# Kernel optimization log

Measured on AMD Instinct MI355X. Metric: run time of the kernel, lower is better.

## Reference

```python
import jax, jax.numpy as jnp
import numpy as np

EPS = 1e-11

def squash(s, axis=-1):
    sq = jnp.sum(s * s, axis=axis, keepdims=True)
    return (sq / (1.0 + sq)) * s / jnp.sqrt(sq + EPS)

def routing(u_hat, scale, num_iters=3):
    # u_hat: (b, P, J, D); dynamic routing (Sabour et al.), softmax over output capsules J
    b, P, J, D = u_hat.shape
    b_ij = jnp.zeros((b, P, J), u_hat.dtype)
    v = None
    for _ in range(num_iters):
        c = jax.nn.softmax(b_ij, axis=-1)
        s = jnp.einsum('bpj,bpjd->bjd', c, u_hat) / scale
        v = squash(s)
        b_ij = b_ij + jnp.einsum('bpjd,bjd->bpj', u_hat, v)
    return v

def normalize_adj(adj):
    deg = jnp.sum(adj, axis=-1)
    d_inv_sqrt = jnp.where(deg > 0, deg ** -0.5, 0.0)
    return d_inv_sqrt[:, :, None] * adj * d_inv_sqrt[:, None, :]

def setup_inputs():
    key = jax.random.key(0)
    ks = jax.random.split(key, 20)
    b, n = 32, 512
    vocabs = [128, 64, 16]
    emb, C, L = 64, 2, 3
    hidden = emb * C                 # 128
    gcn_in = emb * len(vocabs)       # 192
    att_dim = emb * C * L            # 384
    Jg, Dg = 16, 32                  # num_graph_capsules, graph_embedding_size
    ncls = 6
    recon_hidden = int(gcn_in * 2 / 3)  # 128
    recon_dim = 208
    g = lambda i, *s: jax.random.normal(ks[i], s, jnp.float32) * 0.05
    # sparse symmetric adjacency with self-loops (binary, like real graph data)
    adj = (jax.random.uniform(ks[0], (b, n, n)) < 0.02).astype(jnp.float32)
    adj = jnp.maximum(adj, jnp.swapaxes(adj, 1, 2))
    adj = jnp.maximum(adj, jnp.eye(n, dtype=jnp.float32)[None])
    return {
        'adj': adj,
        'nodes0': jax.random.randint(ks[1], (b, n), 0, vocabs[0]),
        'nodes1': jax.random.randint(ks[2], (b, n), 0, vocabs[1]),
        'nodes2': jax.random.randint(ks[3], (b, n), 0, vocabs[2]),
        'label': jax.random.randint(ks[4], (b,), 0, ncls),
        'reconstructs': jax.random.uniform(ks[5], (b, recon_dim)),
        'emb0': g(6, vocabs[0], emb), 'emb1': g(7, vocabs[1], emb), 'emb2': g(8, vocabs[2], emb),
        'gw0': g(9, gcn_in, hidden), 'gb0': jnp.zeros((hidden,), jnp.float32),
        'gw1': g(10, hidden, hidden), 'gb1': jnp.zeros((hidden,), jnp.float32),
        'gw2': g(11, hidden, hidden), 'gb2': jnp.zeros((hidden,), jnp.float32),
        'aw1': g(12, att_dim, att_dim), 'ab1': jnp.zeros((att_dim,), jnp.float32),
        'aw2': g(13, att_dim, 1), 'ab2': jnp.zeros((1,), jnp.float32),
        'Wg': g(14, C * L, emb, Jg, Dg),
        'Wc': g(15, Jg, Dg, ncls, Dg),
        'rw1': g(16, Dg, recon_hidden), 'rb1': jnp.zeros((recon_hidden,), jnp.float32),
        'rw2': g(17, recon_hidden, recon_dim), 'rb2': jnp.zeros((recon_dim,), jnp.float32),
    }

def reference(adj, nodes0, nodes1, nodes2, label, reconstructs,
              emb0, emb1, emb2, gw0, gb0, gw1, gb1, gw2, gb2,
              aw1, ab1, aw2, ab2, Wg, Wc, rw1, rb1, rw2, rb2):
    b, n, _ = adj.shape
    C = 2
    lambda_val, reg_scale = 0.5, 0.1
    # embeddings (dropout omitted: eval-mode reference)
    feats = jnp.concatenate([emb0[nodes0], emb1[nodes1], emb2[nodes2]], axis=-1)  # (b,n,192)
    masks = jnp.max(adj, axis=-1, keepdims=True)                    # (b,n,1)
    num_nodes = jnp.sum(masks, axis=1, keepdims=True)[..., None]    # (b,1,1,1)
    adj_norm = normalize_adj(adj)
    hid = []
    h = feats
    for W, bb in ((gw0, gb0), (gw1, gb1), (gw2, gb2)):
        h = jnp.tanh(jnp.einsum('bnm,bmd->bnd', adj_norm, h @ W + bb))
        hid.append(h.reshape(b, n, C, -1))
    H = jnp.concatenate(hid, axis=2)                                # (b,n,C*L,emb)
    attn = jnp.tanh(H.reshape(b, n, -1) @ aw1 + ab1) @ aw2 + ab2    # (b,n,1)
    attn = jax.nn.softmax(jnp.where(masks > 0, attn, -jnp.inf), axis=1)[..., None]
    H = H * attn * num_nodes
    # graph capsules: every (node, channel) is an input capsule
    Jg, Dg = Wg.shape[2], Wg.shape[3]
    u_hat = jnp.einsum('bnci,cijd->bncjd', H, Wg).reshape(b, n * Wg.shape[0], Jg, Dg)
    v_g = routing(u_hat, num_nodes.reshape(b, 1, 1))                # (b,Jg,Dg)
    u_hat2 = jnp.einsum('bci,cijd->bcjd', v_g, Wc)
    v_c = routing(u_hat2, 1.0)                                      # (b,ncls,Dg)
    # margin loss
    v_mag = jnp.sqrt(jnp.sum(v_c * v_c, axis=2))
    pred = jnp.argmax(v_mag, axis=1)
    max_l = jnp.maximum(0.9 - v_mag, 0.0) ** 2
    max_r = jnp.maximum(v_mag - 0.1, 0.0) ** 2
    T_c = jax.nn.one_hot(label, v_mag.shape[1], dtype=v_c.dtype)
    L_c = jnp.sum(T_c * max_l + lambda_val * (1.0 - T_c) * max_r, axis=1)
    margin_loss = jnp.mean(L_c)
    # reconstruction loss
    capsule_masked = jnp.sum(v_c * T_c[..., None], axis=1)          # (b,Dg)
    rec = jax.nn.sigmoid(jax.nn.relu(capsule_masked @ rw1 + rb1) @ rw2 + rb2)
    neg_ind = (reconstructs < 1e-05).astype(rec.dtype)
    pos_ind = 1.0 - neg_ind
    rec_val = reconstructs / (jnp.max(reconstructs, axis=1, keepdims=True) + EPS)
    diff = (rec - rec_val) ** 2
    recon_loss = jnp.mean(jnp.max(diff * pos_ind, axis=-1) + jnp.max(diff * neg_ind, axis=-1))
    loss = margin_loss + recon_loss * reg_scale
    return (v_c, loss, margin_loss, recon_loss, pred)
```

## Files before the change

### kernel.cpp

```cpp
#include <hip/hip_runtime.h>
#include <hip/hip_bf16.h>
#include <math.h>

#define NB 32
#define NN 512
#define GIN 192
#define ATT 384
#define EPSF 1e-11f

typedef __attribute__((ext_vector_type(4))) float f32x4;
typedef __attribute__((ext_vector_type(8))) short short8;

__device__ __forceinline__ ushort bfhi(float f) {
    uint u = __float_as_uint(f);
    return (ushort)((u + 0x7FFFu + ((u >> 16) & 1u)) >> 16);
}
__device__ __forceinline__ float bff(ushort h) {
    return __uint_as_float(((uint)h) << 16);
}
__device__ __forceinline__ void bfsplit(float f, ushort& hi, ushort& lo) {
    hi = bfhi(f);
    lo = bfhi(f - bff(hi));
}

__global__ __launch_bounds__(64) void k_prep(const float* __restrict__ adj,
                                             ushort* __restrict__ nbr,
                                             int* __restrict__ deg,
                                             float* __restrict__ dinv,
                                             float* __restrict__ mask) {
    int row = blockIdx.x;
    int t = threadIdx.x;
    const float* a = adj + (size_t)row * NN;
    float4 v0 = ((const float4*)a)[t * 2];
    float4 v1 = ((const float4*)a)[t * 2 + 1];
    float vv[8] = {v0.x, v0.y, v0.z, v0.w, v1.x, v1.y, v1.z, v1.w};
    float s = 0.f, m = 0.f;
    int cnt = 0;
    unsigned long long below = (t == 63) ? 0xFFFFFFFFFFFFFFFFULL >> 1
                                         : ((1ULL << t) - 1ULL);
#pragma unroll
    for (int e = 0; e < 8; e++) {
        float v = vv[e];
        s += v;
        m = fmaxf(m, v);
        bool nz = v != 0.f;
        unsigned long long bm = __ballot(nz);
        int pos = cnt + __popcll(bm & below);
        if (nz && pos < 64) nbr[(size_t)row * 64 + pos] = (ushort)(t * 8 + e);
        cnt += __popcll(bm);
    }
    for (int off = 32; off; off >>= 1) {
        s += __shfl_xor(s, off);
        m = fmaxf(m, __shfl_xor(m, off));
    }
    if (t == 0) {
        deg[row] = cnt < 64 ? cnt : 64;
        dinv[row] = s > 0.f ? 1.0f / sqrtf(s) : 0.f;
        mask[row] = m;
    }
}

__global__ void k_gather(const int* __restrict__ n0, const int* __restrict__ n1,
                         const int* __restrict__ n2, const float* __restrict__ e0,
                         const float* __restrict__ e1, const float* __restrict__ e2,
                         ushort* __restrict__ fh, ushort* __restrict__ fl) {
    int tid = blockIdx.x * 256 + threadIdx.x;
    if (tid >= NB * NN * GIN) return;
    int bn = tid / GIN, f = tid - bn * GIN;
    float v;
    if (f < 64)       v = e0[n0[bn] * 64 + f];
    else if (f < 128) v = e1[n1[bn] * 64 + (f - 64)];
    else              v = e2[n2[bn] * 64 + (f - 128)];
    ushort h, lo;
    bfsplit(v, h, lo);
    fh[tid] = h; fl[tid] = lo;
}

__global__ __launch_bounds__(256) void k_twtall(
    const float* __restrict__ gw0, const float* __restrict__ gw1,
    const float* __restrict__ gw2, const float* __restrict__ aw1,
    ushort* __restrict__ t0h, ushort* __restrict__ t0l,
    ushort* __restrict__ t1h, ushort* __restrict__ t1l,
    ushort* __restrict__ t2h, ushort* __restrict__ t2l,
    ushort* __restrict__ tah, ushort* __restrict__ tal) {
    const float* W; ushort *Th, *Tl; int K, N;
    switch (blockIdx.z) {
        case 0: W = gw0; Th = t0h; Tl = t0l; K = 192; N = 128; break;
        case 1: W = gw1; Th = t1h; Tl = t1l; K = 128; N = 128; break;
        case 2: W = gw2; Th = t2h; Tl = t2l; K = 128; N = 128; break;
        default: W = aw1; Th = tah; Tl = tal; K = 384; N = 384; break;
    }
    int k0 = blockIdx.x * 32, n0 = blockIdx.y * 32;
    if (k0 >= K || n0 >= N) return;
    __shared__ float tile[32][33];
    int t = threadIdx.x, tx = t & 31, ty = t >> 5;
#pragma unroll
    for (int r = 0; r < 4; r++)
        tile[ty + r * 8][tx] = W[(size_t)(k0 + ty + r * 8) * N + n0 + tx];
    __syncthreads();
#pragma unroll
    for (int r = 0; r < 4; r++) {
        int nn = ty + r * 8;
        float v = tile[tx][nn];
        ushort h, lo;
        bfsplit(v, h, lo);
        size_t o = (size_t)(n0 + nn) * K + k0 + tx;
        Th[o] = h; Tl[o] = lo;
    }
}

template <int KK, int EPI>
__global__ __launch_bounds__(256) void k_mfg(
    const ushort* __restrict__ Ah, const ushort* __restrict__ Al, int lda,
    const ushort* __restrict__ Bh, const ushort* __restrict__ Bl,
    const float* __restrict__ bias, const float* __restrict__ dinv,
    ushort* __restrict__ O1, ushort* __restrict__ O2, float* __restrict__ Of,
    const float* __restrict__ aw2p) {
    __shared__ ushort Ash[2048], Asl[2048];
    __shared__ ushort Bsh[4096], Bsl[4096];
    __shared__ float ep[(EPI == 0) ? 64 * 128 : 1];
    int t = threadIdx.x;
    int bid = blockIdx.x;
    {
        int q = gridDim.x >> 3;
        bid = (bid & 7) * q + (bid >> 3);
    }
    int m0 = bid * 64;
    int n0 = blockIdx.y * 128;
    int l = t & 63, w = t >> 6, wr = w >> 1, wc = w & 1;
    int rA = t >> 2, kc = t & 3;
    int rB0 = rA, rB1 = rA + 64;
    int lsA  = ((rA >> 4) * 64 + (rA & 15) + kc * 16) * 8;
    int lsB0 = ((rB0 >> 4) * 64 + (rB0 & 15) + kc * 16) * 8;
    int lsB1 = ((rB1 >> 4) * 64 + (rB1 & 15) + kc * 16) * 8;
    f32x4 z = {0.f, 0.f, 0.f, 0.f};
    f32x4 acc[2][4];
#pragma unroll
    for (int i = 0; i < 2; i++)
#pragma unroll
        for (int j = 0; j < 4; j++) acc[i][j] = z;

    short8 pa0, pal0, pb0, pb1, pbl0, pbl1;
    int kof = kc * 8;
    {
        pa0 = *(const short8*)&Ah[(size_t)(m0 + rA) * lda + kof];
        pal0 = *(const short8*)&Al[(size_t)(m0 + rA) * lda + kof];
        pb0 = *(const short8*)&Bh[(size_t)(n0 + rB0) * KK + kof];
        pb1 = *(const short8*)&Bh[(size_t)(n0 + rB1) * KK + kof];
        pbl0 = *(const short8*)&Bl[(size_t)(n0 + rB0) * KK + kof];
        pbl1 = *(const short8*)&Bl[(size_t)(n0 + rB1) * KK + kof];
    }
    for (int k0 = 0; k0 < KK; k0 += 32) {
        *(short8*)&Ash[lsA] = pa0;
        *(short8*)&Asl[lsA] = pal0;
        *(short8*)&Bsh[lsB0] = pb0;
        *(short8*)&Bsh[lsB1] = pb1;
        *(short8*)&Bsl[lsB0] = pbl0;
        *(short8*)&Bsl[lsB1] = pbl1;
        __syncthreads();
        if (k0 + 32 < KK) {
            int kn = k0 + 32 + kof;
            pa0 = *(const short8*)&Ah[(size_t)(m0 + rA) * lda + kn];
            pal0 = *(const short8*)&Al[(size_t)(m0 + rA) * lda + kn];
            pb0 = *(const short8*)&Bh[(size_t)(n0 + rB0) * KK + kn];
            pb1 = *(const short8*)&Bh[(size_t)(n0 + rB1) * KK + kn];
            pbl0 = *(const short8*)&Bl[(size_t)(n0 + rB0) * KK + kn];
            pbl1 = *(const short8*)&Bl[(size_t)(n0 + rB1) * KK + kn];
        }
        short8 ah[2], al[2], bh[4], bl[4];
#pragma unroll
        for (int i = 0; i < 2; i++) {
            ah[i] = *(const short8*)&Ash[((wr * 2 + i) * 64 + l) * 8];
            al[i] = *(const short8*)&Asl[((wr * 2 + i) * 64 + l) * 8];
        }
#pragma unroll
        for (int j = 0; j < 4; j++) {
            bh[j] = *(const short8*)&Bsh[((wc * 4 + j) * 64 + l) * 8];
            bl[j] = *(const short8*)&Bsl[((wc * 4 + j) * 64 + l) * 8];
        }
#pragma unroll
        for (int i = 0; i < 2; i++)
#pragma unroll
            for (int j = 0; j < 4; j++) {
                acc[i][j] = __builtin_amdgcn_mfma_f32_16x16x32_bf16(ah[i], bh[j], acc[i][j], 0, 0, 0);
                acc[i][j] = __builtin_amdgcn_mfma_f32_16x16x32_bf16(ah[i], bl[j], acc[i][j], 0, 0, 0);
                acc[i][j] = __builtin_amdgcn_mfma_f32_16x16x32_bf16(al[i], bh[j], acc[i][j], 0, 0, 0);
            }
        __syncthreads();
    }
    if constexpr (EPI == 3) {
#pragma unroll
        for (int i = 0; i < 2; i++) {
            float rs[4] = {0.f, 0.f, 0.f, 0.f};
#pragma unroll
            for (int j = 0; j < 4; j++) {
                int gc = n0 + (wc * 4 + j) * 16 + (l & 15);
                float bv = bias[gc], wv = aw2p[gc];
#pragma unroll
                for (int r = 0; r < 4; r++)
                    rs[r] += tanhf(acc[i][j][r] + bv) * wv;
            }
#pragma unroll
            for (int r = 0; r < 4; r++) {
                rs[r] += __shfl_xor(rs[r], 1, 16);
                rs[r] += __shfl_xor(rs[r], 2, 16);
                rs[r] += __shfl_xor(rs[r], 4, 16);
                rs[r] += __shfl_xor(rs[r], 8, 16);
            }
            if ((l & 15) == 0) {
                int gr0 = m0 + (wr * 2 + i) * 16 + 4 * (l >> 4);
#pragma unroll
                for (int r = 0; r < 4; r++) atomicAdd(&Of[gr0 + r], rs[r]);
            }
        }
    } else {
#pragma unroll
        for (int i = 0; i < 2; i++)
#pragma unroll
            for (int j = 0; j < 4; j++) {
                int lc = (wc * 4 + j) * 16 + (l & 15);
                int lr0 = (wr * 2 + i) * 16 + 4 * (l >> 4);
                float bv = bias[lc];
#pragma unroll
                for (int r = 0; r < 4; r++)
                    ep[(lr0 + r) * 128 + lc] = (acc[i][j][r] + bv) * dinv[m0 + lr0 + r];
            }
        __syncthreads();
        int row = t >> 2, c0 = (t & 3) * 32;
        ushort hs[32], lsv[32];
#pragma unroll
        for (int c = 0; c < 32; c++) bfsplit(ep[row * 128 + c0 + c], hs[c], lsv[c]);
        size_t ob = (size_t)(m0 + row) * 128 + c0;
#pragma unroll
        for (int k = 0; k < 4; k++) {
            *(short8*)&O1[ob + k * 8] = *(const short8*)&hs[k * 8];
            *(short8*)&O2[ob + k * 8] = *(const short8*)&lsv[k * 8];
        }
    }
}

__global__ __launch_bounds__(256) void k_adjsp(const ushort* __restrict__ nbr,
                                               const int* __restrict__ deg,
                                               const ushort* __restrict__ Yh,
                                               const ushort* __restrict__ Yl,
                                               const float* __restrict__ dinv,
                                               ushort* __restrict__ Hbh,
                                               ushort* __restrict__ Hbl, int hoff) {
    int bid = blockIdx.x;
    {
        int q = gridDim.x >> 3;
        bid = (bid & 7) * q + (bid >> 3);
    }
    int b = bid >> 3, rb = bid & 7;
    int base = b * NN + rb * 64;
    __shared__ ushort nl[64 * 64];
    __shared__ int dl[64];
    int t = threadIdx.x;
    *(short8*)&nl[t * 16] = *(const short8*)&nbr[(size_t)base * 64 + t * 16];
    *(short8*)&nl[t * 16 + 8] = *(const short8*)&nbr[(size_t)base * 64 + t * 16 + 8];
    if (t < 64) dl[t] = deg[base + t];
    __syncthreads();
    int row = t >> 2, c0 = (t & 3) * 32;
    const ushort* yhp = Yh + (size_t)b * 65536 + c0;
    const ushort* ylp = Yl + (size_t)b * 65536 + c0;
    float acc[32];
#pragma unroll
    for (int c = 0; c < 32; c++) acc[c] = 0.f;
    int dg = dl[row];
    for (int q = 0; q < dg; q++) {
        int m = nl[row * 64 + q];
        const short8* yh = (const short8*)(yhp + m * 128);
        const short8* yl = (const short8*)(ylp + m * 128);
        short8 h0 = yh[0], h1 = yh[1], h2 = yh[2], h3 = yh[3];
        short8 l0 = yl[0], l1 = yl[1], l2 = yl[2], l3 = yl[3];
#pragma unroll
        for (int k = 0; k < 8; k++) {
            acc[k]      += bff((ushort)h0[k]) + bff((ushort)l0[k]);
            acc[8 + k]  += bff((ushort)h1[k]) + bff((ushort)l1[k]);
            acc[16 + k] += bff((ushort)h2[k]) + bff((ushort)l2[k]);
            acc[24 + k] += bff((ushort)h3[k]) + bff((ushort)l3[k]);
        }
    }
    float dv = dinv[base + row];
    ushort hs[32], lsv[32];
#pragma unroll
    for (int c = 0; c < 32; c++) {
        float v = tanhf(acc[c] * dv);
        bfsplit(v, hs[c], lsv[c]);
    }
    size_t o = (size_t)(base + row) * ATT + hoff + c0;
#pragma unroll
    for (int k = 0; k < 4; k++) {
        *(short8*)&Hbh[o + k * 8] = *(const short8*)&hs[k * 8];
        *(short8*)&Hbl[o + k * 8] = *(const short8*)&lsv[k * 8];
    }
}

__global__ __launch_bounds__(512) void k_attnsm(float* __restrict__ logit,
                                                const float* __restrict__ mask,
                                                float* __restrict__ numn) {
    __shared__ float red[8], red2[8], red3[8];
    int b = blockIdx.x, t = threadIdx.x;
    float mk = mask[b * NN + t];
    float x = mk > 0.f ? logit[b * NN + t] : -INFINITY;
    float m = x, nsum = mk;
    for (int off = 32; off; off >>= 1) {
        m = fmaxf(m, __shfl_xor(m, off));
        nsum += __shfl_xor(nsum, off);
    }
    if ((t & 63) == 0) { red[t >> 6] = m; red3[t >> 6] = nsum; }
    __syncthreads();
    float gm = red[0], nn = red3[0];
    for (int i = 1; i < 8; i++) { gm = fmaxf(gm, red[i]); nn += red3[i]; }
    float e = expf(x - gm);
    float s = e;
    for (int off = 32; off; off >>= 1) s += __shfl_xor(s, off);
    if ((t & 63) == 0) red2[t >> 6] = s;
    __syncthreads();
    float gs = 0.f;
    for (int i = 0; i < 8; i++) gs += red2[i];
    logit[b * NN + t] = (e / gs) * nn;
    if (t == 0) numn[b] = nn;
}

__global__ __launch_bounds__(256) void k_Hsum(const ushort* __restrict__ Hh,
                                              const ushort* __restrict__ Hl,
                                              const float* __restrict__ scale,
                                              float* __restrict__ G0) {
    int blk = blockIdx.x;
    int c = blk % 6, b = blk / 6;
    int t = threadIdx.x;
    int i = t & 63, g = t >> 6;
    float s = 0.f;
    for (int n = g * 128; n < g * 128 + 128; n++) {
        size_t o = ((size_t)b * NN + n) * ATT + c * 64 + i;
        s += scale[b * NN + n] * (bff(Hh[o]) + bff(Hl[o]));
    }
    __shared__ float red[256];
    red[t] = s;
    __syncthreads();
    if (t < 128) red[t] += red[t + 128];
    __syncthreads();
    if (t < 64) G0[(size_t)blk * 64 + i] = red[t] + red[t + 64];
}

template <int SRC, bool DOWV>
__global__ __launch_bounds__(256) void k_SVj(const float* __restrict__ gsrc,
                                             const float* __restrict__ Wg,
                                             const float* __restrict__ numn,
                                             float* __restrict__ vg,
                                             float* __restrict__ Wv) {
    int b = blockIdx.x, j = blockIdx.y;
    int t = threadIdx.x;
    __shared__ float Wgl[384 * 33];
    __shared__ float gj[384];
    __shared__ float red[256];
    __shared__ float vvs[32];
    for (int idx = t; idx < 12288; idx += 256) {
        int r = idx >> 5, d = idx & 31;
        Wgl[r * 33 + d] = Wg[(size_t)r * 512 + j * 32 + d];
    }
    for (int r = t; r < 384; r += 256) {
        if constexpr (SRC == 0) {
            gj[r] = gsrc[b * 384 + r] * (1.f / 16.f);
        } else {
            const float* g = gsrc + ((size_t)b * 6 + (r >> 6)) * 4096 + j * 64 + (r & 63);
            gj[r] = g[0] + g[1024] + g[2048] + g[3072];
        }
    }
    __syncthreads();
    int d = t & 31, g8 = t >> 5;
    float pp = 0.f;
#pragma unroll
    for (int k = 0; k < 48; k++) {
        int r = g8 * 48 + k;
        pp += gj[r] * Wgl[r * 33 + d];
    }
    red[t] = pp;
    __syncthreads();
    if (t < 128) red[t] += red[t + 128];
    __syncthreads();
    if (t < 64) red[t] += red[t + 64];
    __syncthreads();
    if (t < 32) {
        float s = (red[t] + red[t + 32]) / numn[b];
        float sq = s * s;
        for (int off = 16; off; off >>= 1) sq += __shfl_xor(sq, off, 32);
        float v = (sq / (1.f + sq)) * s / sqrtf(sq + EPSF);
        vvs[t] = v;
        vg[(size_t)b * 512 + j * 32 + t] = v;
    }
    __syncthreads();
    if constexpr (DOWV) {
        for (int r = t; r < 384; r += 256) {
            float a = 0.f;
#pragma unroll
            for (int d2 = 0; d2 < 32; d2++) a += Wgl[r * 33 + d2] * vvs[d2];
            Wv[(size_t)b * 6144 + (r >> 6) * 1024 + (r & 63) * 16 + j] = a;
        }
    }
}

__global__ __launch_bounds__(256) void k_GsSM(const float* __restrict__ bij,
                                              const ushort* __restrict__ Hh,
                                              const ushort* __restrict__ Hl,
                                              const float* __restrict__ scale,
                                              float* __restrict__ Gs) {
    int blk = blockIdx.x;
    int seg = blk & 3, c = (blk >> 2) % 6, b = blk / 24;
    __shared__ float ct[16 * 16];
    __shared__ float ht[16 * 64];
    int t = threadIdx.x;
    int i = t & 63, j0 = t >> 6;
    float acc[4] = {0.f, 0.f, 0.f, 0.f};
    int n0 = seg * 128;
    for (int nc = 0; nc < 128; nc += 16) {
        {
            int nn = t >> 4;
            float v = bij[(((size_t)b * NN + n0 + nc + nn) * 6 + c) * 16 + (t & 15)];
            float mx = v;
            mx = fmaxf(mx, __shfl_xor(mx, 1, 16));
            mx = fmaxf(mx, __shfl_xor(mx, 2, 16));
            mx = fmaxf(mx, __shfl_xor(mx, 4, 16));
            mx = fmaxf(mx, __shfl_xor(mx, 8, 16));
            float e = expf(v - mx);
            float sm = e;
            sm += __shfl_xor(sm, 1, 16);
            sm += __shfl_xor(sm, 2, 16);
            sm += __shfl_xor(sm, 4, 16);
            sm += __shfl_xor(sm, 8, 16);
            ct[t] = e / sm;
        }
        for (int idx = t; idx < 1024; idx += 256) {
            int nn = idx >> 6, ii = idx & 63;
            int n = n0 + nc + nn;
            size_t o = ((size_t)b * NN + n) * ATT + c * 64 + ii;
            ht[idx] = scale[b * NN + n] * (bff(Hh[o]) + bff(Hl[o]));
        }
        __syncthreads();
        for (int nn = 0; nn < 16; nn++) {
            float hv = ht[nn * 64 + i];
#pragma unroll
            for (int q = 0; q < 4; q++) acc[q] += ct[nn * 16 + j0 * 4 + q] * hv;
        }
        __syncthreads();
    }
#pragma unroll
    for (int q = 0; q < 4; q++) {
        int j = j0 * 4 + q;
        Gs[(((size_t)b * 6 + c) * 4 + seg) * 1024 + j * 64 + i] = acc[q];
    }
}

template <bool ACC>
__global__ __launch_bounds__(256) void k_bup(const ushort* __restrict__ Hh,
                                             const ushort* __restrict__ Hl,
                                             const float* __restrict__ scale,
                                             const float* __restrict__ Wv,
                                             float* __restrict__ bij) {
    int blk = blockIdx.x;
    int b = blk >> 4;
    int n0 = (blk & 15) * 32;
    __shared__ float wl[6144];
    __shared__ float hl[32 * ATT];
    int t = threadIdx.x;
    for (int idx = t; idx < 6144; idx += 256) wl[idx] = Wv[(size_t)b * 6144 + idx];
    for (int idx = t; idx < 32 * ATT; idx += 256) {
        int nn = idx / ATT;
        size_t o = ((size_t)b * NN + n0) * ATT + idx;
        hl[idx] = scale[b * NN + n0 + nn] * (bff(Hh[o]) + bff(Hl[o]));
    }
    __syncthreads();
    for (int idx = t; idx < 3072; idx += 256) {
        int nn = idx / 96, r = idx % 96, c = r >> 4, j = r & 15;
        float a = 0.f;
        const float* h = hl + nn * ATT + c * 64;
        const float* w = wl + c * 1024 + j;
#pragma unroll
        for (int i2 = 0; i2 < 64; i2++) a += h[i2] * w[i2 * 16];
        size_t o = (((size_t)b * NN + n0 + nn) * 6 + c) * 16 + j;
        if constexpr (ACC) bij[o] += a;
        else bij[o] = a;
    }
}

__global__ __launch_bounds__(256) void k_u2(const float* __restrict__ vg,
                                            const float* __restrict__ Wc,
                                            float* __restrict__ u2g) {
    int c = blockIdx.x;
    int t = threadIdx.x;
    __shared__ float Wcl[32 * 192];
    __shared__ float vgl[32 * 32];
    for (int idx = t; idx < 6144; idx += 256)
        Wcl[idx] = Wc[(size_t)c * 6144 + idx];
    for (int idx = t; idx < 1024; idx += 256) {
        int b = idx >> 5, i2 = idx & 31;
        vgl[idx] = vg[(size_t)b * 512 + c * 32 + i2];
    }
    __syncthreads();
    for (int o = t; o < 6144; o += 256) {
        int b = o / 192, jd = o - b * 192;
        float a = 0.f;
#pragma unroll
        for (int i2 = 0; i2 < 32; i2++) a += vgl[b * 32 + i2] * Wcl[i2 * 192 + jd];
        u2g[(size_t)b * 3072 + c * 192 + jd] = a;
    }
}

__global__ __launch_bounds__(256) void k_caps2(
    const float* __restrict__ u2g,
    const int* __restrict__ label, const float* __restrict__ recon_in,
    const float* __restrict__ rw1, const float* __restrict__ rb1,
    const float* __restrict__ rw2, const float* __restrict__ rb2,
    float* __restrict__ out, float* __restrict__ marg, float* __restrict__ reconl) {
    int b = blockIdx.x, t = threadIdx.x;
    __shared__ float u2[3072];
    __shared__ float b2[96], c2b[96];
    __shared__ float vv[192];
    __shared__ float magl[6];
    __shared__ float cm[32];
    __shared__ float hidl[128];
    __shared__ float red[256];
    for (int idx = t; idx < 3072; idx += 256) u2[idx] = u2g[(size_t)b * 3072 + idx];
    if (t < 96) b2[t] = 0.f;
    __syncthreads();
    for (int it = 0; it < 3; it++) {
        if (t < 16) {
            float mx = -INFINITY;
            for (int j = 0; j < 6; j++) mx = fmaxf(mx, b2[t * 6 + j]);
            float e[6], s = 0.f;
            for (int j = 0; j < 6; j++) { e[j] = expf(b2[t * 6 + j] - mx); s += e[j]; }
            for (int j = 0; j < 6; j++) c2b[t * 6 + j] = e[j] / s;
        }
        __syncthreads();
        if (t < 192) {
            int j = t >> 5, d = t & 31;
            float s = 0.f;
            for (int c = 0; c < 16; c++) s += c2b[c * 6 + j] * u2[c * 192 + j * 32 + d];
            float sq = s * s;
            for (int off = 16; off; off >>= 1) sq += __shfl_xor(sq, off, 32);
            vv[t] = (sq / (1.f + sq)) * s / sqrtf(sq + EPSF);
        }
        __syncthreads();
        if (it < 2) {
            if (t < 96) {
                int c = t / 6, j = t - c * 6;
                float a = 0.f;
                for (int d = 0; d < 32; d++) a += u2[c * 192 + j * 32 + d] * vv[j * 32 + d];
                b2[t] += a;
            }
            __syncthreads();
        }
    }
    if (t < 192) out[(size_t)b * 192 + t] = vv[t];
    if (t < 6) {
        float s = 0.f;
        for (int d = 0; d < 32; d++) { float v = vv[t * 32 + d]; s += v * v; }
        magl[t] = sqrtf(s);
    }
    __syncthreads();
    int lab = label[b];
    if (t == 0) {
        float L = 0.f;
        int p = 0;
        float best = magl[0];
        for (int j = 0; j < 6; j++) {
            float mg = magl[j];
            if (mg > best) { best = mg; p = j; }
            float ml = fmaxf(0.9f - mg, 0.f); ml *= ml;
            float mr = fmaxf(mg - 0.1f, 0.f); mr *= mr;
            L += (j == lab) ? ml : 0.5f * mr;
        }
        marg[b] = L;
        out[6147 + b] = (float)p;
    }
    if (t < 32) cm[t] = vv[lab * 32 + t];
    __syncthreads();
    if (t < 128) {
        float a = rb1[t];
        for (int d = 0; d < 32; d++) a += cm[d] * rw1[d * 128 + t];
        hidl[t] = fmaxf(a, 0.f);
    }
    __syncthreads();
    bool act = t < 208;
    float rv = 0.f, rin = 0.f;
    if (act) {
        float a = rb2[t];
        for (int k = 0; k < 128; k++) a += hidl[k] * rw2[k * 208 + t];
        rv = 1.f / (1.f + expf(-a));
        rin = recon_in[(size_t)b * 208 + t];
    }
    red[t] = act ? rin : -INFINITY;
    __syncthreads();
    for (int s2 = 128; s2; s2 >>= 1) {
        if (t < s2) red[t] = fmaxf(red[t], red[t + s2]);
        __syncthreads();
    }
    float rmax = red[0];
    __syncthreads();
    float dpos = 0.f, dneg = 0.f;
    if (act) {
        float rec_val = rin / (rmax + EPSF);
        float d2 = rv - rec_val; d2 *= d2;
        bool neg = rin < 1e-5f;
        dpos = neg ? 0.f : d2;
        dneg = neg ? d2 : 0.f;
    }
    red[t] = dpos;
    __syncthreads();
    for (int s2 = 128; s2; s2 >>= 1) {
        if (t < s2) red[t] = fmaxf(red[t], red[t + s2]);
        __syncthreads();
    }
    float mp = red[0];
    __syncthreads();
    red[t] = dneg;
    __syncthreads();
    for (int s2 = 128; s2; s2 >>= 1) {
        if (t < s2) red[t] = fmaxf(red[t], red[t + s2]);
        __syncthreads();
    }
    if (t == 0) reconl[b] = mp + red[0];
}

__global__ void k_final(const float* __restrict__ marg, const float* __restrict__ reconl,
                        float* __restrict__ out) {
    int t = threadIdx.x;
    float m = (t < 32) ? marg[t] : 0.f;
    float r = (t < 32) ? reconl[t] : 0.f;
    for (int off = 16; off; off >>= 1) { m += __shfl_xor(m, off, 32); r += __shfl_xor(r, off, 32); }
    if (t == 0) {
        m /= 32.f;
        r /= 32.f;
        out[6144] = m + 0.1f * r;
        out[6145] = m;
        out[6146] = r;
    }
}

extern "C" void kernel_launch(void* const* d_in, const int* in_sizes, int n_in,
                              void* d_out, int out_size, void* d_ws, size_t ws_size,
                              hipStream_t stream) {
    const float* adj   = (const float*)d_in[0];
    const int*   n0    = (const int*)d_in[1];
    const int*   n1    = (const int*)d_in[2];
    const int*   n2    = (const int*)d_in[3];
    const int*   label = (const int*)d_in[4];
    const float* recon = (const float*)d_in[5];
    const float* e0    = (const float*)d_in[6];
    const float* e1    = (const float*)d_in[7];
    const float* e2    = (const float*)d_in[8];
    const float* gw0   = (const float*)d_in[9];
    const float* gb0   = (const float*)d_in[10];
    const float* gw1   = (const float*)d_in[11];
    const float* gb1   = (const float*)d_in[12];
    const float* gw2   = (const float*)d_in[13];
    const float* gb2   = (const float*)d_in[14];
    const float* aw1   = (const float*)d_in[15];
    const float* ab1   = (const float*)d_in[16];
    const float* aw2   = (const float*)d_in[17];
    const float* Wg    = (const float*)d_in[19];
    const float* Wc    = (const float*)d_in[20];
    const float* rw1   = (const float*)d_in[21];
    const float* rb1   = (const float*)d_in[22];
    const float* rw2   = (const float*)d_in[23];
    const float* rb2   = (const float*)d_in[24];
    float* out = (float*)d_out;

    char* p = (char*)d_ws;
    auto alloc = [&](size_t bytes) { char* r = p; p += (bytes + 255) & ~(size_t)255; return r; };
    float*  dinv   = (float*)alloc(NB * NN * 4);
    float*  maskp  = (float*)alloc(NB * NN * 4);
    float*  numn   = (float*)alloc(NB * 4);
    float*  logit  = (float*)alloc(NB * NN * 4);
    float*  bij    = (float*)alloc((size_t)NB * NN * 96 * 4);
    float*  Gs     = (float*)alloc((size_t)NB * 24576 * 4);
    float*  G0     = (float*)alloc(NB * 384 * 4);
    float*  vg     = (float*)alloc(NB * 512 * 4);
    float*  Wv     = (float*)alloc(NB * 6144 * 4);
    float*  u2g    = (float*)alloc(NB * 3072 * 4);
    float*  marg   = (float*)alloc(NB * 4);
    float*  recl   = (float*)alloc(NB * 4);
    int*    deg    = (int*)alloc(NB * NN * 4);
    ushort* nbr    = (ushort*)alloc((size_t)NB * NN * 64 * 2);
    ushort* gwt0h  = (ushort*)alloc(128 * 192 * 2);
    ushort* gwt0l  = (ushort*)alloc(128 * 192 * 2);
    ushort* gwt1h  = (ushort*)alloc(128 * 128 * 2);
    ushort* gwt1l  = (ushort*)alloc(128 * 128 * 2);
    ushort* gwt2h  = (ushort*)alloc(128 * 128 * 2);
    ushort* gwt2l  = (ushort*)alloc(128 * 128 * 2);
    ushort* aw1th  = (ushort*)alloc(384 * 384 * 2);
    ushort* aw1tl  = (ushort*)alloc(384 * 384 * 2);
    ushort* Yth    = (ushort*)alloc((size_t)NB * NN * 128 * 2);
    ushort* Ytl    = (ushort*)alloc((size_t)NB * NN * 128 * 2);
    ushort* Hbh    = (ushort*)alloc((size_t)NB * NN * ATT * 2);
    ushort* Hbl    = (ushort*)alloc((size_t)NB * NN * ATT * 2);
    ushort* fbh    = (ushort*)alloc((size_t)NB * NN * GIN * 2);
    ushort* fbl    = (ushort*)alloc((size_t)NB * NN * GIN * 2);

    k_prep<<<NB * NN, 64, 0, stream>>>(adj, nbr, deg, dinv, maskp);
    k_gather<<<(NB * NN * GIN + 255) / 256, 256, 0, stream>>>(n0, n1, n2, e0, e1, e2, fbh, fbl);
    k_twtall<<<dim3(12, 12, 4), 256, 0, stream>>>(gw0, gw1, gw2, aw1, gwt0h, gwt0l,
                                                  gwt1h, gwt1l, gwt2h, gwt2l, aw1th, aw1tl);

    k_mfg<192, 0><<<256, 256, 0, stream>>>(fbh, fbl, 192, gwt0h, gwt0l, gb0, dinv,
                                           Yth, Ytl, nullptr, nullptr);
    k_adjsp<<<256, 256, 0, stream>>>(nbr, deg, Yth, Ytl, dinv, Hbh, Hbl, 0);
    k_mfg<128, 0><<<256, 256, 0, stream>>>(Hbh, Hbl, ATT, gwt1h, gwt1l, gb1, dinv,
                                           Yth, Ytl, nullptr, nullptr);
    k_adjsp<<<256, 256, 0, stream>>>(nbr, deg, Yth, Ytl, dinv, Hbh, Hbl, 128);
    k_mfg<128, 0><<<256, 256, 0, stream>>>(Hbh + 128, Hbl + 128, ATT, gwt2h, gwt2l, gb2, dinv,
                                           Yth, Ytl, nullptr, nullptr);
    k_adjsp<<<256, 256, 0, stream>>>(nbr, deg, Yth, Ytl, dinv, Hbh, Hbl, 256);

    hipMemsetAsync(logit, 0, NB * NN * sizeof(float), stream);
    k_mfg<384, 3><<<dim3(256, 3), 256, 0, stream>>>(Hbh, Hbl, ATT, aw1th, aw1tl, ab1, nullptr,
                                                    nullptr, nullptr, logit, aw2);
    k_attnsm<<<NB, 512, 0, stream>>>(logit, maskp, numn);

    k_Hsum<<<NB * 6, 256, 0, stream>>>(Hbh, Hbl, logit, G0);
    k_SVj<0, true><<<dim3(NB, 16), 256, 0, stream>>>(G0, Wg, numn, vg, Wv);
    k_bup<false><<<NB * 16, 256, 0, stream>>>(Hbh, Hbl, logit, Wv, bij);
    k_GsSM<<<NB * 24, 256, 0, stream>>>(bij, Hbh, Hbl, logit, Gs);
    k_SVj<1, true><<<dim3(NB, 16), 256, 0, stream>>>(Gs, Wg, numn, vg, Wv);
    k_bup<true><<<NB * 16, 256, 0, stream>>>(Hbh, Hbl, logit, Wv, bij);
    k_GsSM<<<NB * 24, 256, 0, stream>>>(bij, Hbh, Hbl, logit, Gs);
    k_SVj<1, false><<<dim3(NB, 16), 256, 0, stream>>>(Gs, Wg, numn, vg, nullptr);

    k_u2<<<16, 256, 0, stream>>>(vg, Wc, u2g);
    k_caps2<<<NB, 256, 0, stream>>>(u2g, label, recon, rw1, rb1, rw2, rb2, out, marg, recl);
    k_final<<<1, 64, 0, stream>>>(marg, recl, out);
}
```

Before: 440.3 us.

## Store GCN intermediate Y as fp32 and re-split sparse aggregation into finer blocks

The GEMM epilogue now writes the intermediate Y directly as fp32 instead of splitting it into bf16 hi/lo pairs, and the sparse adjacency aggregation reads one fp32 array instead of two bf16 arrays. The aggregation kernel is also re-partitioned into 16 rows per block with 16 threads per row and 8 columns each, quadrupling the grid to 1024 blocks. This removes split/recombine arithmetic, gives each gather coalesced 32-byte reads per thread, and adds parallelism to hide gather latency. The byte count of Y is unchanged, and the smaller blocks reload neighbor lists per block.

```diff
diff --git a/kernel.cpp b/kernel.cpp
--- a/kernel.cpp
+++ b/kernel.cpp
@@ -114,8 +114,7 @@
     const ushort* __restrict__ Ah, const ushort* __restrict__ Al, int lda,
     const ushort* __restrict__ Bh, const ushort* __restrict__ Bl,
     const float* __restrict__ bias, const float* __restrict__ dinv,
-    ushort* __restrict__ O1, ushort* __restrict__ O2, float* __restrict__ Of,
-    const float* __restrict__ aw2p) {
+    float* __restrict__ Of, const float* __restrict__ aw2p) {
     __shared__ ushort Ash[2048], Asl[2048];
     __shared__ ushort Bsh[4096], Bsl[4096];
     __shared__ float ep[(EPI == 0) ? 64 * 128 : 1];
@@ -227,22 +226,16 @@
             }
         __syncthreads();
         int row = t >> 2, c0 = (t & 3) * 32;
-        ushort hs[32], lsv[32];
-#pragma unroll
-        for (int c = 0; c < 32; c++) bfsplit(ep[row * 128 + c0 + c], hs[c], lsv[c]);
         size_t ob = (size_t)(m0 + row) * 128 + c0;
 #pragma unroll
-        for (int k = 0; k < 4; k++) {
-            *(short8*)&O1[ob + k * 8] = *(const short8*)&hs[k * 8];
-            *(short8*)&O2[ob + k * 8] = *(const short8*)&lsv[k * 8];
-        }
+        for (int k = 0; k < 8; k++)
+            ((float4*)&Of[ob])[k] = *(const float4*)&ep[row * 128 + c0 + k * 4];
     }
 }
 
 __global__ __launch_bounds__(256) void k_adjsp(const ushort* __restrict__ nbr,
                                                const int* __restrict__ deg,
-                                               const ushort* __restrict__ Yh,
-                                               const ushort* __restrict__ Yl,
+                                               const float* __restrict__ Y,
                                                const float* __restrict__ dinv,
                                                ushort* __restrict__ Hbh,
                                                ushort* __restrict__ Hbl, int hoff) {
@@ -251,49 +244,38 @@
         int q = gridDim.x >> 3;
         bid = (bid & 7) * q + (bid >> 3);
     }
-    int b = bid >> 3, rb = bid & 7;
-    int base = b * NN + rb * 64;
-    __shared__ ushort nl[64 * 64];
-    __shared__ int dl[64];
-    int t = threadIdx.x;
-    *(short8*)&nl[t * 16] = *(const short8*)&nbr[(size_t)base * 64 + t * 16];
-    *(short8*)&nl[t * 16 + 8] = *(const short8*)&nbr[(size_t)base * 64 + t * 16 + 8];
-    if (t < 64) dl[t] = deg[base + t];
-    __syncthreads();
-    int row = t >> 2, c0 = (t & 3) * 32;
-    const ushort* yhp = Yh + (size_t)b * 65536 + c0;
-    const ushort* ylp = Yl + (size_t)b * 65536 + c0;
-    float acc[32];
-#pragma unroll
-    for (int c = 0; c < 32; c++) acc[c] = 0.f;
+    int b = bid >> 5;
+    int rg = bid & 31;
+    int base = b * NN + rg * 16;
+    __shared__ ushort nl[16 * 64];
+    __shared__ int dl[16];
+    int t = threadIdx.x;
+    if (t < 128) *(short8*)&nl[t * 8] = *(const short8*)&nbr[(size_t)base * 64 + t * 8];
+    if (t < 16) dl[t] = deg[base + t];
+    __syncthreads();
+    int row = t >> 4, c0 = (t & 15) * 8;
+    const float* yp = Y + (size_t)b * 65536 + c0;
+    float acc[8] = {0.f, 0.f, 0.f, 0.f, 0.f, 0.f, 0.f, 0.f};
     int dg = dl[row];
+    const ushort* nr = &nl[row * 64];
     for (int q = 0; q < dg; q++) {
-        int m = nl[row * 64 + q];
-        const short8* yh = (const short8*)(yhp + m * 128);
-        const short8* yl = (const short8*)(ylp + m * 128);
-        short8 h0 = yh[0], h1 = yh[1], h2 = yh[2], h3 = yh[3];
-        short8 l0 = yl[0], l1 = yl[1], l2 = yl[2], l3 = yl[3];
-#pragma unroll
-        for (int k = 0; k < 8; k++) {
-            acc[k]      += bff((ushort)h0[k]) + bff((ushort)l0[k]);
-            acc[8 + k]  += bff((ushort)h1[k]) + bff((ushort)l1[k]);
-            acc[16 + k] += bff((ushort)h2[k]) + bff((ushort)l2[k]);
-            acc[24 + k] += bff((ushort)h3[k]) + bff((ushort)l3[k]);
-        }
+        const float4* y = (const float4*)(yp + (int)nr[q] * 128);
+        float4 a = y[0], c = y[1];
+        acc[0] += a.x; acc[1] += a.y; acc[2] += a.z; acc[3] += a.w;
+        acc[4] += c.x; acc[5] += c.y; acc[6] += c.z; acc[7] += c.w;
     }
     float dv = dinv[base + row];
-    ushort hs[32], lsv[32];
-#pragma unroll
-    for (int c = 0; c < 32; c++) {
+    short8 vh, vl;
+#pragma unroll
+    for (int c = 0; c < 8; c++) {
         float v = tanhf(acc[c] * dv);
-        bfsplit(v, hs[c], lsv[c]);
+        ushort h, lo;
+        bfsplit(v, h, lo);
+        vh[c] = (short)h; vl[c] = (short)lo;
     }
     size_t o = (size_t)(base + row) * ATT + hoff + c0;
-#pragma unroll
-    for (int k = 0; k < 4; k++) {
-        *(short8*)&Hbh[o + k * 8] = *(const short8*)&hs[k * 8];
-        *(short8*)&Hbl[o + k * 8] = *(const short8*)&lsv[k * 8];
-    }
+    *(short8*)&Hbh[o] = vh;
+    *(short8*)&Hbl[o] = vl;
 }
 
 __global__ __launch_bounds__(512) void k_attnsm(float* __restrict__ logit,
@@ -691,8 +673,7 @@
     ushort* gwt2l  = (ushort*)alloc(128 * 128 * 2);
     ushort* aw1th  = (ushort*)alloc(384 * 384 * 2);
     ushort* aw1tl  = (ushort*)alloc(384 * 384 * 2);
-    ushort* Yth    = (ushort*)alloc((size_t)NB * NN * 128 * 2);
-    ushort* Ytl    = (ushort*)alloc((size_t)NB * NN * 128 * 2);
+    float*  Ybuf   = (float*)alloc((size_t)NB * NN * 128 * 4);
     ushort* Hbh    = (ushort*)alloc((size_t)NB * NN * ATT * 2);
     ushort* Hbl    = (ushort*)alloc((size_t)NB * NN * ATT * 2);
     ushort* fbh    = (ushort*)alloc((size_t)NB * NN * GIN * 2);
@@ -703,19 +684,16 @@
     k_twtall<<<dim3(12, 12, 4), 256, 0, stream>>>(gw0, gw1, gw2, aw1, gwt0h, gwt0l,
                                                   gwt1h, gwt1l, gwt2h, gwt2l, aw1th, aw1tl);
 
-    k_mfg<192, 0><<<256, 256, 0, stream>>>(fbh, fbl, 192, gwt0h, gwt0l, gb0, dinv,
-                                           Yth, Ytl, nullptr, nullptr);
-    k_adjsp<<<256, 256, 0, stream>>>(nbr, deg, Yth, Ytl, dinv, Hbh, Hbl, 0);
-    k_mfg<128, 0><<<256, 256, 0, stream>>>(Hbh, Hbl, ATT, gwt1h, gwt1l, gb1, dinv,
-                                           Yth, Ytl, nullptr, nullptr);
-    k_adjsp<<<256, 256, 0, stream>>>(nbr, deg, Yth, Ytl, dinv, Hbh, Hbl, 128);
-    k_mfg<128, 0><<<256, 256, 0, stream>>>(Hbh + 128, Hbl + 128, ATT, gwt2h, gwt2l, gb2, dinv,
-                                           Yth, Ytl, nullptr, nullptr);
-    k_adjsp<<<256, 256, 0, stream>>>(nbr, deg, Yth, Ytl, dinv, Hbh, Hbl, 256);
+    k_mfg<192, 0><<<256, 256, 0, stream>>>(fbh, fbl, 192, gwt0h, gwt0l, gb0, dinv, Ybuf, nullptr);
+    k_adjsp<<<1024, 256, 0, stream>>>(nbr, deg, Ybuf, dinv, Hbh, Hbl, 0);
+    k_mfg<128, 0><<<256, 256, 0, stream>>>(Hbh, Hbl, ATT, gwt1h, gwt1l, gb1, dinv, Ybuf, nullptr);
+    k_adjsp<<<1024, 256, 0, stream>>>(nbr, deg, Ybuf, dinv, Hbh, Hbl, 128);
+    k_mfg<128, 0><<<256, 256, 0, stream>>>(Hbh + 128, Hbl + 128, ATT, gwt2h, gwt2l, gb2, dinv, Ybuf, nullptr);
+    k_adjsp<<<1024, 256, 0, stream>>>(nbr, deg, Ybuf, dinv, Hbh, Hbl, 256);
 
     hipMemsetAsync(logit, 0, NB * NN * sizeof(float), stream);
     k_mfg<384, 3><<<dim3(256, 3), 256, 0, stream>>>(Hbh, Hbl, ATT, aw1th, aw1tl, ab1, nullptr,
-                                                    nullptr, nullptr, logit, aw2);
+                                                    logit, aw2);
     k_attnsm<<<NB, 512, 0, stream>>>(logit, maskp, numn);
 
     k_Hsum<<<NB * 6, 256, 0, stream>>>(Hbh, Hbl, logit, G0);
```

Result: faster. 414.3 us (-5.9%).
